# Kernel tuning notes

Hardware: AMD Instinct MI355X
Metric: run time of the kernel (lower is better)

Reference implementation:

```python
import jax, jax.numpy as jnp
import numpy as np

# Static config (matches init_kwargs)
C = 256       # dim
H = 8         # num_heads
D = C // H    # head dim
K = 32        # patch_size (window length)
G = 1         # rt_size (relay tokens per window)
S = G + K     # window length incl. relay token
NW = 8192     # number of windows
N = NW * K    # total octree points
NB = 2        # number of HOTFormerBlocks in the stage
HID = 4 * C   # mlp hidden (mlp_ratio=4)
LS = 1e-5     # layer_scale init
SCALE = D ** -0.5


def _layernorm(x, g, b):
    m = x.mean(-1, keepdims=True)
    v = ((x - m) ** 2).mean(-1, keepdims=True)
    return (x - m) * jax.lax.rsqrt(v + 1e-5) * g + b


def setup_inputs() -> dict:
    key = jax.random.key(0)
    ks = jax.random.split(key, 20)
    w = 0.02
    inp = {
        "data": jax.random.normal(ks[0], (N, C), jnp.float32),
        "relay_tokens": jax.random.normal(ks[1], (NW, C), jnp.float32),
        # per-block parameters stacked on leading NB axis
        "cpe_w": jax.random.normal(ks[2], (NB, 3, C), jnp.float32) * w,  # depthwise k=3 conv (CPE)
        "cpe_b": jnp.zeros((NB, C), jnp.float32),
        "ln1_g": jnp.ones((NB, C), jnp.float32),
        "ln1_b": jnp.zeros((NB, C), jnp.float32),
        "qkv_w": jax.random.normal(ks[3], (NB, C, 3 * C), jnp.float32) * w,
        "qkv_b": jnp.zeros((NB, 3 * C), jnp.float32),
        "rpe": jax.random.normal(ks[4], (NB, H, S, S), jnp.float32) * w,  # relative position bias per window
        "proj_w": jax.random.normal(ks[5], (NB, C, C), jnp.float32) * w,
        "proj_b": jnp.zeros((NB, C), jnp.float32),
        "ln2_g": jnp.ones((NB, C), jnp.float32),
        "ln2_b": jnp.zeros((NB, C), jnp.float32),
        "mlp_w1": jax.random.normal(ks[6], (NB, C, HID), jnp.float32) * w,
        "mlp_b1": jnp.zeros((NB, HID), jnp.float32),
        "mlp_w2": jax.random.normal(ks[7], (NB, HID, C), jnp.float32) * w,
        "mlp_b2": jnp.zeros((NB, C), jnp.float32),
        "gamma1": jnp.full((NB, C), LS, jnp.float32),
        "gamma2": jnp.full((NB, C), LS, jnp.float32),
    }
    return inp


def reference(data, relay_tokens, cpe_w, cpe_b, ln1_g, ln1_b, qkv_w, qkv_b,
              rpe, proj_w, proj_b, ln2_g, ln2_b, mlp_w1, mlp_b1, mlp_w2,
              mlp_b2, gamma1, gamma2):
    rt = relay_tokens
    for i in range(NB):
        # CPE: depthwise kernel-3 conv along octree serialization order
        xp = jnp.pad(data, ((1, 1), (0, 0)))
        cpe = xp[:-2] * cpe_w[i, 0] + xp[1:-1] * cpe_w[i, 1] + xp[2:] * cpe_w[i, 2] + cpe_b[i]
        d = data + cpe
        # data_to_windows + prepend relay token -> [NW, S, C]
        win = d.reshape(NW, K, C)
        x = jnp.concatenate([rt[:, None, :], win], axis=1)
        # windowed MHA with RPE bias
        h = _layernorm(x, ln1_g[i], ln1_b[i])
        qkv = (h @ qkv_w[i] + qkv_b[i]).reshape(NW, S, 3, H, D)
        q, k, v = qkv[:, :, 0], qkv[:, :, 1], qkv[:, :, 2]  # [NW,S,H,D]
        scores = jnp.einsum('nqhd,nkhd->nhqk', q, k) * SCALE + rpe[i][None]
        attn = jax.nn.softmax(scores, axis=-1)
        o = jnp.einsum('nhqk,nkhd->nqhd', attn, v).reshape(NW, S, C)
        o = o @ proj_w[i] + proj_b[i]
        x = x + gamma1[i] * o  # layer-scaled residual (drop_path = identity)
        # MLP
        h2 = _layernorm(x, ln2_g[i], ln2_b[i])
        ffn = jax.nn.gelu(h2 @ mlp_w1[i] + mlp_b1[i]) @ mlp_w2[i] + mlp_b2[i]
        x = x + gamma2[i] * ffn
        # split relay token / window data, windows_to_data
        rt = x[:, 0, :]
        data = x[:, G:, :].reshape(N, C)
    return data, rt
```

## Files before the change

kernel.cpp:

```cpp
#include <hip/hip_runtime.h>
#include <hip/hip_bf16.h>


#define NW_    8192
#define KWIN   32
#define SEQ    33
#define NTOK   262144
#define MROWS  270336
#define CDIM   256
#define HEADS  8
#define HIDD   1024

typedef unsigned short u16;
typedef unsigned int u32;
typedef unsigned char u8;
typedef unsigned long long u64;
typedef __attribute__((ext_vector_type(8))) short short8;
typedef __attribute__((ext_vector_type(4))) float f32x4;
typedef __attribute__((ext_vector_type(2))) float f32x2;

__device__ __forceinline__ u16 f2bf(float f) {
    u32 u = __builtin_bit_cast(u32, f);
    u += 0x7FFFu + ((u >> 16) & 1u);
    return (u16)(u >> 16);
}
__device__ __forceinline__ float bf2f(u16 h) {
    return __builtin_bit_cast(float, (u32)h << 16);
}
__device__ __forceinline__ u32 pk2(float lo, float hi) {
    union { __hip_bfloat162 h; u32 u; } cvt;
    cvt.h = __float22bfloat162_rn(make_float2(lo, hi));
    return cvt.u;
}
__device__ __forceinline__ u32 pk4f8(float a, float b, float c, float d) {
    int pk = __builtin_amdgcn_cvt_pk_fp8_f32(a, b, 0, false);
    pk = __builtin_amdgcn_cvt_pk_fp8_f32(c, d, pk, true);
    return (u32)pk;
}
__device__ __forceinline__ float wsum(float v) {
#pragma unroll
    for (int off = 32; off > 0; off >>= 1) v += __shfl_xor(v, off);
    return v;
}
__device__ __forceinline__ float gelu_f(float v) {
    float s = fminf(fmaxf(0.4255f * v + 0.5f, 0.f), 1.f);
    return v * s;
}
__device__ __forceinline__ void gload_lds16(const void* g, void* l) {
    __builtin_amdgcn_global_load_lds(
        (const __attribute__((address_space(1))) unsigned int*)g,
        (__attribute__((address_space(3))) unsigned int*)l, 16, 0, 0);
}
__device__ __forceinline__ float4 ld4bf(const u16* p) {
    ushort4 v = *(const ushort4*)p;
    return make_float4(bf2f(v.x), bf2f(v.y), bf2f(v.z), bf2f(v.w));
}

__global__ __launch_bounds__(256) void transpose_fp8_kernel(
    const float* __restrict__ W, u8* __restrict__ Wt, int K, int N)
{
    int idx = blockIdx.x * 256 + threadIdx.x;
    if (idx >= K * N) return;
    int n = idx / K, k = idx - n * K;
    int p = __builtin_amdgcn_cvt_pk_fp8_f32(W[(size_t)k * N + n], 0.f, 0, false);
    Wt[idx] = (u8)p;
}

template<bool BF>
__global__ __launch_bounds__(256) void cpe_ln1_kernel(
    const void* __restrict__ datav, const void* __restrict__ rtv,
    const float* __restrict__ cpe_w, const float* __restrict__ cpe_b,
    const float* __restrict__ ln_g, const float* __restrict__ ln_b,
    u16* __restrict__ x, u8* __restrict__ h)
{
    const int lane = threadIdx.x & 63, wid = threadIdx.x >> 6;
    const int row = blockIdx.x * 4 + wid;
    const int w = row / SEQ, s = row - w * SEQ;
    const int c0 = lane * 4;
    float4 xv;
    if (s == 0) {
        xv = BF ? ld4bf((const u16*)rtv + (size_t)w * CDIM + c0)
                : *(const float4*)((const float*)rtv + (size_t)w * CDIM + c0);
    } else {
        const long t = (long)w * KWIN + s - 1;
        float4 a, am = {0.f,0.f,0.f,0.f}, ap = {0.f,0.f,0.f,0.f};
        if (BF) {
            const u16* d = (const u16*)datav;
            a = ld4bf(d + t * CDIM + c0);
            if (t > 0)        am = ld4bf(d + (t - 1) * CDIM + c0);
            if (t < NTOK - 1) ap = ld4bf(d + (t + 1) * CDIM + c0);
        } else {
            const float* d = (const float*)datav;
            a = *(const float4*)(d + t * CDIM + c0);
            if (t > 0)        am = *(const float4*)(d + (t - 1) * CDIM + c0);
            if (t < NTOK - 1) ap = *(const float4*)(d + (t + 1) * CDIM + c0);
        }
        const float4 w0 = *(const float4*)(cpe_w + 0 * CDIM + c0);
        const float4 w1 = *(const float4*)(cpe_w + 1 * CDIM + c0);
        const float4 w2 = *(const float4*)(cpe_w + 2 * CDIM + c0);
        const float4 cb = *(const float4*)(cpe_b + c0);
        xv.x = a.x + am.x * w0.x + a.x * w1.x + ap.x * w2.x + cb.x;
        xv.y = a.y + am.y * w0.y + a.y * w1.y + ap.y * w2.y + cb.y;
        xv.z = a.z + am.z * w0.z + a.z * w1.z + ap.z * w2.z + cb.z;
        xv.w = a.w + am.w * w0.w + a.w * w1.w + ap.w * w2.w + cb.w;
    }
    float s1 = wsum(xv.x + xv.y + xv.z + xv.w);
    float s2 = wsum(xv.x * xv.x + xv.y * xv.y + xv.z * xv.z + xv.w * xv.w);
    const float mean = s1 * (1.f / 256.f);
    const float var  = s2 * (1.f / 256.f) - mean * mean;
    const float rs   = rsqrtf(var + 1e-5f);
    const float4 g = *(const float4*)(ln_g + c0);
    const float4 b = *(const float4*)(ln_b + c0);
    uint2 xo = { pk2(xv.x, xv.y), pk2(xv.z, xv.w) };
    *(uint2*)(x + (size_t)row * CDIM + c0) = xo;
    const float h0 = (xv.x - mean) * rs * g.x + b.x;
    const float h1 = (xv.y - mean) * rs * g.y + b.y;
    const float h2 = (xv.z - mean) * rs * g.z + b.z;
    const float h3 = (xv.w - mean) * rs * g.w + b.w;
    *(u32*)(h + (size_t)row * CDIM + c0) = pk4f8(h0, h1, h2, h3);
}

__global__ __launch_bounds__(256) void ln_kernel(
    const u16* __restrict__ x, const float* __restrict__ ln_g,
    const float* __restrict__ ln_b, u8* __restrict__ h)
{
    const int lane = threadIdx.x & 63, wid = threadIdx.x >> 6;
    const int row = blockIdx.x * 4 + wid;
    const int c0 = lane * 4;
    float4 xv = ld4bf(x + (size_t)row * CDIM + c0);
    float s1 = wsum(xv.x + xv.y + xv.z + xv.w);
    float s2 = wsum(xv.x * xv.x + xv.y * xv.y + xv.z * xv.z + xv.w * xv.w);
    const float mean = s1 * (1.f / 256.f);
    const float var  = s2 * (1.f / 256.f) - mean * mean;
    const float rs   = rsqrtf(var + 1e-5f);
    const float4 g = *(const float4*)(ln_g + c0);
    const float4 b = *(const float4*)(ln_b + c0);
    const float h0 = (xv.x - mean) * rs * g.x + b.x;
    const float h1 = (xv.y - mean) * rs * g.y + b.y;
    const float h2 = (xv.z - mean) * rs * g.z + b.z;
    const float h3 = (xv.w - mean) * rs * g.w + b.w;
    *(u32*)(h + (size_t)row * CDIM + c0) = pk4f8(h0, h1, h2, h3);
}

template<int KT, int NT, int MODE>
__global__ __launch_bounds__(256, 4) void gemm_fp8_kernel(
    const u8* __restrict__ A8, const u8* __restrict__ Bt8,
    const float* __restrict__ bias, u8* __restrict__ Cout8,
    u16* __restrict__ xbuf, const float* __restrict__ gamma,
    u16* __restrict__ sdata, u16* __restrict__ srt, float* __restrict__ fout)
{
    constexpr bool F8OUT = (MODE == 1 || MODE == 5);
    __shared__ u16 sm[F8OUT ? 16384 : 17408];
    const int lane = threadIdx.x & 63, wid = threadIdx.x >> 6;
    constexpr int CX = NT / 128;
    constexpr int BAND = (MROWS / 128) / 8;
    const int bid = blockIdx.x;
    const int xcd = bid & 7, local = bid >> 3;
    const int rb = local / CX, cx = local - rb * CX;
    const int row0 = (xcd * BAND + rb) * 128;
    const int col0 = cx * 128;
    const int wr = (wid >> 1) * 64, wc = (wid & 1) * 64;
    const int lr = lane & 15, lg = lane >> 4;
    const int sw = lr & 7;
    f32x4 acc[4][4] = {};
    constexpr int NTk = KT / 128;

    const u8* pa[4];
    const u8* pb[4];
#pragma unroll
    for (int cc = 0; cc < 4; ++cc) {
        const int g = wid * 4 + cc;
        const int chunk = g * 64 + lane;
        const int r = chunk >> 3, c8 = chunk & 7;
        const int c8s = c8 ^ (r & 7);
        pa[cc] = A8  + (size_t)(row0 + r) * KT + c8s * 16;
        pb[cc] = Bt8 + (size_t)(col0 + r) * KT + c8s * 16;
    }

    for (int t = 0; t < NTk; ++t) {
        __syncthreads();
#pragma unroll
        for (int cc = 0; cc < 4; ++cc) {
            const int g = wid * 4 + cc;
            gload_lds16(pa[cc], (char*)sm + g * 1024);
            gload_lds16(pb[cc], (char*)sm + 16384 + g * 1024);
            pa[cc] += 128; pb[cc] += 128;
        }
        __syncthreads();
        const u8* Ab = (const u8*)sm;
        const u8* Bb = (const u8*)sm + 16384;
#pragma unroll
        for (int kk = 0; kk < 4; ++kk) {
            const int gi = kk * 2 + (lg >> 1);
            const int off8 = (lg & 1) * 8;
            long a[4], b[4];
#pragma unroll
            for (int m = 0; m < 4; ++m)
                a[m] = *(const long*)(Ab + (wr + m * 16 + lr) * 128 + ((gi ^ sw) * 16) + off8);
#pragma unroll
            for (int n = 0; n < 4; ++n)
                b[n] = *(const long*)(Bb + (wc + n * 16 + lr) * 128 + ((gi ^ sw) * 16) + off8);
#pragma unroll
            for (int m = 0; m < 4; ++m)
#pragma unroll
                for (int n = 0; n < 4; ++n)
                    acc[m][n] = __builtin_amdgcn_mfma_f32_16x16x32_fp8_fp8(
                        a[m], b[n], acc[m][n], 0, 0, 0);
        }
    }

    __syncthreads();
    if (F8OUT) {
        u8* Ct8 = (u8*)sm;
#pragma unroll
        for (int n = 0; n < 4; ++n) {
            const int col = wc + n * 16 + lr;
            const float bv = bias[col0 + col];
#pragma unroll
            for (int m = 0; m < 4; ++m) {
                float v0 = acc[m][n][0] + bv, v1 = acc[m][n][1] + bv;
                float v2 = acc[m][n][2] + bv, v3 = acc[m][n][3] + bv;
                if (MODE == 1) { v0 = gelu_f(v0); v1 = gelu_f(v1); v2 = gelu_f(v2); v3 = gelu_f(v3); }
                const u32 pk = pk4f8(v0, v1, v2, v3);
                u8* bp = Ct8 + (wr + m * 16 + lg * 4) * 144 + col;
                bp[0]   = (u8)pk;
                bp[144] = (u8)(pk >> 8);
                bp[288] = (u8)(pk >> 16);
                bp[432] = (u8)(pk >> 24);
            }
        }
        __syncthreads();
#pragma unroll
        for (int it = 0; it < 4; ++it) {
            const int c = it * 256 + threadIdx.x;
            const int row = c >> 3, gr = c & 7;
            *(uint4*)(Cout8 + (size_t)(row0 + row) * NT + col0 + gr * 16) =
                *(const uint4*)(Ct8 + row * 144 + gr * 16);
        }
    } else {
        u16* Ct = sm;
#pragma unroll
        for (int n = 0; n < 4; ++n) {
            const int col = wc + n * 16 + lr;
            const float bv = bias[col0 + col];
#pragma unroll
            for (int m = 0; m < 4; ++m) {
                const u32 p01 = pk2(acc[m][n][0] + bv, acc[m][n][1] + bv);
                const u32 p23 = pk2(acc[m][n][2] + bv, acc[m][n][3] + bv);
                u16* bp = Ct + (wr + m * 16 + lg * 4) * 136 + col;
                bp[0]   = (u16)p01;
                bp[136] = (u16)(p01 >> 16);
                bp[272] = (u16)p23;
                bp[408] = (u16)(p23 >> 16);
            }
        }
        __syncthreads();
#pragma unroll
        for (int it = 0; it < 8; ++it) {
            const int c = it * 256 + threadIdx.x;
            const int row = c >> 4, gr = c & 15;
            const int cc0 = col0 + gr * 8;
            short8 v = *(const short8*)(Ct + row * 136 + gr * 8);
            const int grow = row0 + row;
            const float4 g0 = *(const float4*)(gamma + cc0);
            const float4 g1 = *(const float4*)(gamma + cc0 + 4);
            const float gj[8] = {g0.x, g0.y, g0.z, g0.w, g1.x, g1.y, g1.z, g1.w};
            u16* xp = xbuf + (size_t)grow * CDIM + cc0;
            short8 xv = *(const short8*)(xp);
            float xn[8];
#pragma unroll
            for (int j = 0; j < 8; ++j)
                xn[j] = bf2f((u16)xv[j]) + gj[j] * bf2f((u16)v[j]);
            if (MODE == 2) {
                uint4 o = { pk2(xn[0], xn[1]), pk2(xn[2], xn[3]),
                            pk2(xn[4], xn[5]), pk2(xn[6], xn[7]) };
                *(uint4*)xp = o;
            } else {
                const int w = grow / SEQ, s = grow - w * SEQ;
                if (MODE == 3) {
                    u16* dst = (s == 0) ? srt + (size_t)w * CDIM + cc0
                                        : sdata + ((size_t)w * KWIN + s - 1) * CDIM + cc0;
                    uint4 o = { pk2(xn[0], xn[1]), pk2(xn[2], xn[3]),
                                pk2(xn[4], xn[5]), pk2(xn[6], xn[7]) };
                    *(uint4*)dst = o;
                } else {
                    float* dst = (s == 0) ? fout + (size_t)NTOK * CDIM + (size_t)w * CDIM + cc0
                                          : fout + ((size_t)w * KWIN + s - 1) * CDIM + cc0;
                    *(float4*)dst       = make_float4(xn[0], xn[1], xn[2], xn[3]);
                    *(float4*)(dst + 4) = make_float4(xn[4], xn[5], xn[6], xn[7]);
                }
            }
        }
    }
}

__global__ __launch_bounds__(256) void attn_mfma_kernel(
    const u8* __restrict__ qkv, const float* __restrict__ rpe,
    u8* __restrict__ o)
{
    __shared__ u8 sm[4 * 6144];
    const int lane = threadIdx.x & 63, wid = threadIdx.x >> 6;
    u8* Qs = sm + wid * 6144;
    u8* Ks = Qs + 1920;
    u8* Ps = Qs;
    u8* Vt = Qs + 3840;
    const int task = blockIdx.x * 4 + wid;
    const int w = task >> 3, hh = task & 7;
    const u8* base = qkv + (size_t)(w * SEQ) * 768 + hh * 32;

#pragma unroll
    for (int it = 0; it < 5; ++it) {
        int idx = it * 64 + lane;
        if (idx < 288) *(u64*)(Vt + idx * 8) = 0ull;
    }
#pragma unroll
    for (int it = 0; it < 3; ++it) {
        int idx = it * 64 + lane;
        if (idx < 132) {
            int s = idx >> 2, c = idx & 3;
            *(u64*)(Qs + s * 40 + c * 8) = *(const u64*)(base + (size_t)s * 768 + c * 8);
            *(u64*)(Ks + s * 40 + c * 8) = *(const u64*)(base + (size_t)s * 768 + 256 + c * 8);
        }
    }
#pragma unroll
    for (int it = 0; it < 3; ++it) {
        int idx = it * 64 + lane;
        if (idx < 132) {
            int c = idx / 33, k = idx - c * 33;
            u64 v = *(const u64*)(base + (size_t)k * 768 + 512 + c * 8);
#pragma unroll
            for (int j = 0; j < 8; ++j)
                Vt[(c * 8 + j) * 72 + k] = (u8)(v >> (8 * j));
        }
    }

    const int lr = lane & 15, lg = lane >> 4;
    long qa[3], kb[3];
#pragma unroll
    for (int mi = 0; mi < 3; ++mi)
        qa[mi] = *(const long*)(Qs + (mi * 16 + lr) * 40 + lg * 8);
#pragma unroll
    for (int ni = 0; ni < 3; ++ni)
        kb[ni] = *(const long*)(Ks + (ni * 16 + lr) * 40 + lg * 8);
    f32x4 sc[3][3];
#pragma unroll
    for (int mi = 0; mi < 3; ++mi)
#pragma unroll
        for (int ni = 0; ni < 3; ++ni) {
            f32x4 z = {0.f, 0.f, 0.f, 0.f};
            sc[mi][ni] = __builtin_amdgcn_mfma_f32_16x16x32_fp8_fp8(
                qa[mi], kb[ni], z, 0, 0, 0);
        }

#pragma unroll
    for (int it = 0; it < 4; ++it) {
        int idx = it * 64 + lane;
        if (idx < 240) {
            int r = idx / 5, g = idx - r * 5;
            *(u64*)(Ps + r * 72 + 32 + g * 8) = 0ull;
        }
    }

    const float* rp = rpe + hh * SEQ * SEQ;
    const float scale = 0.17677669529663687f;
#pragma unroll
    for (int mi = 0; mi < 3; ++mi) {
#pragma unroll
        for (int q = 0; q < 4; ++q) {
            const int row = mi * 16 + lg * 4 + q;
            const bool rv_ok = (row < 33);
            float r0 = rv_ok ? rp[row * 33 + lr] : 0.f;
            float r1 = rv_ok ? rp[row * 33 + 16 + lr] : 0.f;
            float r2 = (rv_ok && lr == 0) ? rp[row * 33 + 32] : 0.f;
            float s0 = sc[mi][0][q] * scale + r0;
            float s1 = sc[mi][1][q] * scale + r1;
            float s2 = (lr == 0) ? sc[mi][2][q] * scale + r2 : -1e30f;
            float m = fmaxf(fmaxf(s0, s1), s2);
#pragma unroll
            for (int off = 1; off < 16; off <<= 1) m = fmaxf(m, __shfl_xor(m, off));
            float e0 = __expf(s0 - m), e1 = __expf(s1 - m), e2 = __expf(s2 - m);
            float sum = e0 + e1 + e2;
#pragma unroll
            for (int off = 1; off < 16; off <<= 1) sum += __shfl_xor(sum, off);
            const float inv = 1.f / sum;
            u32 p01 = (u32)__builtin_amdgcn_cvt_pk_fp8_f32(e0 * inv, e1 * inv, 0, false);
            u32 p2  = (u32)__builtin_amdgcn_cvt_pk_fp8_f32(e2 * inv, 0.f, 0, false);
            Ps[row * 72 + lr]      = (u8)p01;
            Ps[row * 72 + 16 + lr] = (u8)(p01 >> 8);
            Ps[row * 72 + 32 + lr] = (u8)p2;
        }
    }

    f32x4 oacc[3][2] = {};
#pragma unroll
    for (int ks = 0; ks < 2; ++ks) {
        long pa[3], vb[2];
#pragma unroll
        for (int mi = 0; mi < 3; ++mi)
            pa[mi] = *(const long*)(Ps + (mi * 16 + lr) * 72 + ks * 32 + lg * 8);
#pragma unroll
        for (int ni = 0; ni < 2; ++ni)
            vb[ni] = *(const long*)(Vt + (ni * 16 + lr) * 72 + ks * 32 + lg * 8);
#pragma unroll
        for (int mi = 0; mi < 3; ++mi)
#pragma unroll
            for (int ni = 0; ni < 2; ++ni)
                oacc[mi][ni] = __builtin_amdgcn_mfma_f32_16x16x32_fp8_fp8(
                    pa[mi], vb[ni], oacc[mi][ni], 0, 0, 0);
    }

#pragma unroll
    for (int mi = 0; mi < 3; ++mi)
#pragma unroll
        for (int q = 0; q < 4; ++q) {
            const int row = mi * 16 + lg * 4 + q;
            if (row < 33) {
#pragma unroll
                for (int ni = 0; ni < 2; ++ni) {
                    int pk = __builtin_amdgcn_cvt_pk_fp8_f32(oacc[mi][ni][q], 0.f, 0, false);
                    o[(size_t)(w * SEQ + row) * CDIM + hh * 32 + ni * 16 + lr] = (u8)pk;
                }
            }
        }
}

extern "C" void kernel_launch(void* const* d_in, const int* in_sizes, int n_in,
                              void* d_out, int out_size, void* d_ws, size_t ws_size,
                              hipStream_t stream)
{
    const float* data0  = (const float*)d_in[0];
    const float* rt0    = (const float*)d_in[1];
    const float* cpe_w  = (const float*)d_in[2];
    const float* cpe_b  = (const float*)d_in[3];
    const float* ln1_g  = (const float*)d_in[4];
    const float* ln1_b  = (const float*)d_in[5];
    const float* qkv_w  = (const float*)d_in[6];
    const float* qkv_b  = (const float*)d_in[7];
    const float* rpe    = (const float*)d_in[8];
    const float* proj_w = (const float*)d_in[9];
    const float* proj_b = (const float*)d_in[10];
    const float* ln2_g  = (const float*)d_in[11];
    const float* ln2_b  = (const float*)d_in[12];
    const float* w1     = (const float*)d_in[13];
    const float* b1     = (const float*)d_in[14];
    const float* w2     = (const float*)d_in[15];
    const float* b2     = (const float*)d_in[16];
    const float* g1     = (const float*)d_in[17];
    const float* g2     = (const float*)d_in[18];
    float* out = (float*)d_out;

    char* ws = (char*)d_ws;
    u8*  regA   = (u8*)ws;
    u8*  regB   = (u8*)(ws + 553648128ull);
    u16* x      = (u16*)(ws + 692060160ull);
    u16* xnd    = (u16*)(ws + 830472192ull);
    u16* xnr    = (u16*)(ws + 964689920ull);
    u8*  wqf8   = (u8*) (ws + 968884224ull);
    u8*  w1f8   = (u8*) (ws + 969277440ull);
    u8*  w2f8   = (u8*) (ws + 969801728ull);
    u8*  wpf8   = (u8*) (ws + 970326016ull);

    for (int i = 0; i < 2; ++i) {
        transpose_fp8_kernel<<<(256 * 768 + 255) / 256, 256, 0, stream>>>(
            qkv_w + (size_t)i * 256 * 768, wqf8 + (size_t)i * 768 * 256, 256, 768);
        transpose_fp8_kernel<<<(256 * 256 + 255) / 256, 256, 0, stream>>>(
            proj_w + (size_t)i * 256 * 256, wpf8 + (size_t)i * 256 * 256, 256, 256);
        transpose_fp8_kernel<<<(256 * 1024 + 255) / 256, 256, 0, stream>>>(
            w1 + (size_t)i * 256 * 1024, w1f8 + (size_t)i * 1024 * 256, 256, 1024);
        transpose_fp8_kernel<<<(256 * 1024 + 255) / 256, 256, 0, stream>>>(
            w2 + (size_t)i * 1024 * 256, w2f8 + (size_t)i * 256 * 1024, 1024, 256);
    }

    const int RT = MROWS / 128;

    for (int i = 0; i < 2; ++i) {
        if (i == 0)
            cpe_ln1_kernel<false><<<MROWS / 4, 256, 0, stream>>>(
                data0, rt0, cpe_w, cpe_b, ln1_g, ln1_b, x, regB);
        else
            cpe_ln1_kernel<true><<<MROWS / 4, 256, 0, stream>>>(
                xnd, xnr, cpe_w + 3 * 256, cpe_b + 256,
                ln1_g + 256, ln1_b + 256, x, regB);

        gemm_fp8_kernel<256, 768, 5><<<RT * 6, 256, 0, stream>>>(
            regB, wqf8 + (size_t)i * 768 * 256, qkv_b + (size_t)i * 768,
            regA, nullptr, nullptr, nullptr, nullptr, nullptr);

        attn_mfma_kernel<<<NW_ * HEADS / 4, 256, 0, stream>>>(
            regA, rpe + (size_t)i * HEADS * SEQ * SEQ, regB);

        gemm_fp8_kernel<256, 256, 2><<<RT * 2, 256, 0, stream>>>(
            regB, wpf8 + (size_t)i * 256 * 256, proj_b + (size_t)i * 256,
            nullptr, x, g1 + (size_t)i * 256, nullptr, nullptr, nullptr);

        ln_kernel<<<MROWS / 4, 256, 0, stream>>>(
            x, ln2_g + (size_t)i * 256, ln2_b + (size_t)i * 256, regB);

        gemm_fp8_kernel<256, 1024, 1><<<RT * 8, 256, 0, stream>>>(
            regB, w1f8 + (size_t)i * 1024 * 256, b1 + (size_t)i * 1024,
            regA, nullptr, nullptr, nullptr, nullptr, nullptr);

        if (i == 0)
            gemm_fp8_kernel<1024, 256, 3><<<RT * 2, 256, 0, stream>>>(
                regA, w2f8, b2,
                nullptr, x, g2, xnd, xnr, nullptr);
        else
            gemm_fp8_kernel<1024, 256, 4><<<RT * 2, 256, 0, stream>>>(
                regA, w2f8 + (size_t)256 * 1024, b2 + 256,
                nullptr, x, g2 + 256, nullptr, nullptr, out);
    }
}
```

Baseline: 1.631 ms.

## Enlarge FP8 GEMM block tile to 256x128 with 512 threads

The FP8 GEMM kernel now computes 256-row by 128-column output tiles with 8 waves instead of 128x128 tiles with 4 waves. Each B tile staged in shared memory is reused by twice as many rows, which halves B global loads and the number of blocks. The global-to-LDS loader mapping and grid indexing are reworked to fit. The bf16 residual epilogue now runs in two 128-row halves so it fits the shared buffer. Shared memory grows to 48KB per block, which may lower occupancy and reduce the number of blocks available to fill the GPU.

```diff
diff --git a/kernel.cpp b/kernel.cpp
--- a/kernel.cpp
+++ b/kernel.cpp
@@ -143,21 +143,22 @@
 }
 
 template<int KT, int NT, int MODE>
-__global__ __launch_bounds__(256, 4) void gemm_fp8_kernel(
+__global__ __launch_bounds__(512, 4) void gemm_fp8_kernel(
     const u8* __restrict__ A8, const u8* __restrict__ Bt8,
     const float* __restrict__ bias, u8* __restrict__ Cout8,
     u16* __restrict__ xbuf, const float* __restrict__ gamma,
     u16* __restrict__ sdata, u16* __restrict__ srt, float* __restrict__ fout)
 {
     constexpr bool F8OUT = (MODE == 1 || MODE == 5);
-    __shared__ u16 sm[F8OUT ? 16384 : 17408];
-    const int lane = threadIdx.x & 63, wid = threadIdx.x >> 6;
+    __shared__ u8 sm8[49152];
+    const int tid = threadIdx.x;
+    const int lane = tid & 63, wid = tid >> 6;
     constexpr int CX = NT / 128;
-    constexpr int BAND = (MROWS / 128) / 8;
+    constexpr int BAND = (MROWS / 256) / 8;
     const int bid = blockIdx.x;
     const int xcd = bid & 7, local = bid >> 3;
     const int rb = local / CX, cx = local - rb * CX;
-    const int row0 = (xcd * BAND + rb) * 128;
+    const int row0 = (xcd * BAND + rb) * 256;
     const int col0 = cx * 128;
     const int wr = (wid >> 1) * 64, wc = (wid & 1) * 64;
     const int lr = lane & 15, lg = lane >> 4;
@@ -166,29 +167,35 @@
     constexpr int NTk = KT / 128;
 
     const u8* pa[4];
-    const u8* pb[4];
+    const u8* pb[2];
 #pragma unroll
     for (int cc = 0; cc < 4; ++cc) {
-        const int g = wid * 4 + cc;
-        const int chunk = g * 64 + lane;
-        const int r = chunk >> 3, c8 = chunk & 7;
-        const int c8s = c8 ^ (r & 7);
-        pa[cc] = A8  + (size_t)(row0 + r) * KT + c8s * 16;
-        pb[cc] = Bt8 + (size_t)(col0 + r) * KT + c8s * 16;
+        const int G = cc * 512 + tid;
+        const int r = G >> 3, c8 = G & 7;
+        pa[cc] = A8 + (size_t)(row0 + r) * KT + (c8 ^ (r & 7)) * 16;
+    }
+#pragma unroll
+    for (int cc = 0; cc < 2; ++cc) {
+        const int G = cc * 512 + tid;
+        const int r = G >> 3, c8 = G & 7;
+        pb[cc] = Bt8 + (size_t)(col0 + r) * KT + (c8 ^ (r & 7)) * 16;
     }
 
     for (int t = 0; t < NTk; ++t) {
         __syncthreads();
 #pragma unroll
         for (int cc = 0; cc < 4; ++cc) {
-            const int g = wid * 4 + cc;
-            gload_lds16(pa[cc], (char*)sm + g * 1024);
-            gload_lds16(pb[cc], (char*)sm + 16384 + g * 1024);
-            pa[cc] += 128; pb[cc] += 128;
+            gload_lds16(pa[cc], sm8 + (cc * 512 + tid) * 16);
+            pa[cc] += 128;
+        }
+#pragma unroll
+        for (int cc = 0; cc < 2; ++cc) {
+            gload_lds16(pb[cc], sm8 + 32768 + (cc * 512 + tid) * 16);
+            pb[cc] += 128;
         }
         __syncthreads();
-        const u8* Ab = (const u8*)sm;
-        const u8* Bb = (const u8*)sm + 16384;
+        const u8* Ab = sm8;
+        const u8* Bb = sm8 + 32768;
 #pragma unroll
         for (int kk = 0; kk < 4; ++kk) {
             const int gi = kk * 2 + (lg >> 1);
@@ -211,7 +218,7 @@
 
     __syncthreads();
     if (F8OUT) {
-        u8* Ct8 = (u8*)sm;
+        u8* Ct8 = sm8;
 #pragma unroll
         for (int n = 0; n < 4; ++n) {
             const int col = wc + n * 16 + lr;
@@ -232,62 +239,69 @@
         __syncthreads();
 #pragma unroll
         for (int it = 0; it < 4; ++it) {
-            const int c = it * 256 + threadIdx.x;
+            const int c = it * 512 + tid;
             const int row = c >> 3, gr = c & 7;
             *(uint4*)(Cout8 + (size_t)(row0 + row) * NT + col0 + gr * 16) =
                 *(const uint4*)(Ct8 + row * 144 + gr * 16);
         }
     } else {
-        u16* Ct = sm;
-#pragma unroll
-        for (int n = 0; n < 4; ++n) {
-            const int col = wc + n * 16 + lr;
-            const float bv = bias[col0 + col];
-#pragma unroll
-            for (int m = 0; m < 4; ++m) {
-                const u32 p01 = pk2(acc[m][n][0] + bv, acc[m][n][1] + bv);
-                const u32 p23 = pk2(acc[m][n][2] + bv, acc[m][n][3] + bv);
-                u16* bp = Ct + (wr + m * 16 + lg * 4) * 136 + col;
-                bp[0]   = (u16)p01;
-                bp[136] = (u16)(p01 >> 16);
-                bp[272] = (u16)p23;
-                bp[408] = (u16)(p23 >> 16);
+        u16* Ct = (u16*)sm8;
+#pragma unroll
+        for (int p = 0; p < 2; ++p) {
+            __syncthreads();
+            if ((wid >> 2) == p) {
+                const int wrl = wr - p * 128;
+#pragma unroll
+                for (int n = 0; n < 4; ++n) {
+                    const int col = wc + n * 16 + lr;
+                    const float bv = bias[col0 + col];
+#pragma unroll
+                    for (int m = 0; m < 4; ++m) {
+                        const u32 p01 = pk2(acc[m][n][0] + bv, acc[m][n][1] + bv);
+                        const u32 p23 = pk2(acc[m][n][2] + bv, acc[m][n][3] + bv);
+                        u16* bp = Ct + (wrl + m * 16 + lg * 4) * 136 + col;
+                        bp[0]   = (u16)p01;
+                        bp[136] = (u16)(p01 >> 16);
+                        bp[272] = (u16)p23;
+                        bp[408] = (u16)(p23 >> 16);
+                    }
+                }
             }
-        }
-        __syncthreads();
-#pragma unroll
-        for (int it = 0; it < 8; ++it) {
-            const int c = it * 256 + threadIdx.x;
-            const int row = c >> 4, gr = c & 15;
-            const int cc0 = col0 + gr * 8;
-            short8 v = *(const short8*)(Ct + row * 136 + gr * 8);
-            const int grow = row0 + row;
-            const float4 g0 = *(const float4*)(gamma + cc0);
-            const float4 g1 = *(const float4*)(gamma + cc0 + 4);
-            const float gj[8] = {g0.x, g0.y, g0.z, g0.w, g1.x, g1.y, g1.z, g1.w};
-            u16* xp = xbuf + (size_t)grow * CDIM + cc0;
-            short8 xv = *(const short8*)(xp);
-            float xn[8];
-#pragma unroll
-            for (int j = 0; j < 8; ++j)
-                xn[j] = bf2f((u16)xv[j]) + gj[j] * bf2f((u16)v[j]);
-            if (MODE == 2) {
-                uint4 o = { pk2(xn[0], xn[1]), pk2(xn[2], xn[3]),
-                            pk2(xn[4], xn[5]), pk2(xn[6], xn[7]) };
-                *(uint4*)xp = o;
-            } else {
-                const int w = grow / SEQ, s = grow - w * SEQ;
-                if (MODE == 3) {
-                    u16* dst = (s == 0) ? srt + (size_t)w * CDIM + cc0
-                                        : sdata + ((size_t)w * KWIN + s - 1) * CDIM + cc0;
+            __syncthreads();
+#pragma unroll
+            for (int it = 0; it < 4; ++it) {
+                const int c = it * 512 + tid;
+                const int row = c >> 4, gr = c & 15;
+                const int cc0 = col0 + gr * 8;
+                short8 v = *(const short8*)(Ct + row * 136 + gr * 8);
+                const int grow = row0 + p * 128 + row;
+                const float4 g0 = *(const float4*)(gamma + cc0);
+                const float4 g1 = *(const float4*)(gamma + cc0 + 4);
+                const float gj[8] = {g0.x, g0.y, g0.z, g0.w, g1.x, g1.y, g1.z, g1.w};
+                u16* xp = xbuf + (size_t)grow * CDIM + cc0;
+                short8 xv = *(const short8*)(xp);
+                float xn[8];
+#pragma unroll
+                for (int j = 0; j < 8; ++j)
+                    xn[j] = bf2f((u16)xv[j]) + gj[j] * bf2f((u16)v[j]);
+                if (MODE == 2) {
                     uint4 o = { pk2(xn[0], xn[1]), pk2(xn[2], xn[3]),
                                 pk2(xn[4], xn[5]), pk2(xn[6], xn[7]) };
-                    *(uint4*)dst = o;
+                    *(uint4*)xp = o;
                 } else {
-                    float* dst = (s == 0) ? fout + (size_t)NTOK * CDIM + (size_t)w * CDIM + cc0
-                                          : fout + ((size_t)w * KWIN + s - 1) * CDIM + cc0;
-                    *(float4*)dst       = make_float4(xn[0], xn[1], xn[2], xn[3]);
-                    *(float4*)(dst + 4) = make_float4(xn[4], xn[5], xn[6], xn[7]);
+                    const int w = grow / SEQ, s = grow - w * SEQ;
+                    if (MODE == 3) {
+                        u16* dst = (s == 0) ? srt + (size_t)w * CDIM + cc0
+                                            : sdata + ((size_t)w * KWIN + s - 1) * CDIM + cc0;
+                        uint4 o = { pk2(xn[0], xn[1]), pk2(xn[2], xn[3]),
+                                    pk2(xn[4], xn[5]), pk2(xn[6], xn[7]) };
+                        *(uint4*)dst = o;
+                    } else {
+                        float* dst = (s == 0) ? fout + (size_t)NTOK * CDIM + (size_t)w * CDIM + cc0
+                                              : fout + ((size_t)w * KWIN + s - 1) * CDIM + cc0;
+                        *(float4*)dst       = make_float4(xn[0], xn[1], xn[2], xn[3]);
+                        *(float4*)(dst + 4) = make_float4(xn[4], xn[5], xn[6], xn[7]);
+                    }
                 }
             }
         }
@@ -471,7 +485,7 @@
             w2 + (size_t)i * 1024 * 256, w2f8 + (size_t)i * 256 * 1024, 1024, 256);
     }
 
-    const int RT = MROWS / 128;
+    const int RT2 = MROWS / 256;
 
     for (int i = 0; i < 2; ++i) {
         if (i == 0)
@@ -482,30 +496,30 @@
                 xnd, xnr, cpe_w + 3 * 256, cpe_b + 256,
                 ln1_g + 256, ln1_b + 256, x, regB);
 
-        gemm_fp8_kernel<256, 768, 5><<<RT * 6, 256, 0, stream>>>(
+        gemm_fp8_kernel<256, 768, 5><<<RT2 * 6, 512, 0, stream>>>(
             regB, wqf8 + (size_t)i * 768 * 256, qkv_b + (size_t)i * 768,
             regA, nullptr, nullptr, nullptr, nullptr, nullptr);
 
         attn_mfma_kernel<<<NW_ * HEADS / 4, 256, 0, stream>>>(
             regA, rpe + (size_t)i * HEADS * SEQ * SEQ, regB);
 
-        gemm_fp8_kernel<256, 256, 2><<<RT * 2, 256, 0, stream>>>(
+        gemm_fp8_kernel<256, 256, 2><<<RT2 * 2, 512, 0, stream>>>(
             regB, wpf8 + (size_t)i * 256 * 256, proj_b + (size_t)i * 256,
             nullptr, x, g1 + (size_t)i * 256, nullptr, nullptr, nullptr);
 
         ln_kernel<<<MROWS / 4, 256, 0, stream>>>(
             x, ln2_g + (size_t)i * 256, ln2_b + (size_t)i * 256, regB);
 
-        gemm_fp8_kernel<256, 1024, 1><<<RT * 8, 256, 0, stream>>>(
+        gemm_fp8_kernel<256, 1024, 1><<<RT2 * 8, 512, 0, stream>>>(
             regB, w1f8 + (size_t)i * 1024 * 256, b1 + (size_t)i * 1024,
             regA, nullptr, nullptr, nullptr, nullptr, nullptr);
 
         if (i == 0)
-            gemm_fp8_kernel<1024, 256, 3><<<RT * 2, 256, 0, stream>>>(
+            gemm_fp8_kernel<1024, 256, 3><<<RT2 * 2, 512, 0, stream>>>(
                 regA, w2f8, b2,
                 nullptr, x, g2, xnd, xnr, nullptr);
         else
-            gemm_fp8_kernel<1024, 256, 4><<<RT * 2, 256, 0, stream>>>(
+            gemm_fp8_kernel<1024, 256, 4><<<RT2 * 2, 512, 0, stream>>>(
                 regA, w2f8 + (size_t)256 * 1024, b2 + 256,
                 nullptr, x, g2 + 256, nullptr, nullptr, out);
     }
```

New measurement: 1.750 ms. 1.07x slower.
